# Performance work log

Hardware: AMD Instinct MI355X
Metric: run time of the kernel (lower is better)

The kernel has to match this reference:

```python
import jax, jax.numpy as jnp
import numpy as np
import math

ENC_MAX = 64
DEC_MAX = 128


def _tran_mask(M):
    # faithful reconstruction of self.tran and self.mask buffers
    fs = math.log(DEC_MAX / (DEC_MAX + ENC_MAX))  # fixed_shift_p
    fe = math.log(ENC_MAX / (DEC_MAX + ENC_MAX))  # fixed_emit_p
    i = np.arange(M)[:, None]
    j = np.arange(M)[None, :]
    tran = np.where(i + j < M, (M - (i + j) - 1) * fs + fe, 0.0).astype(np.float32)
    # mask_br: -inf where i+j >= M (anti-diagonal i+j==M-1 stays 0)
    mask = np.where(i + j >= M, -np.inf, 0.0).astype(np.float32)
    return jnp.asarray(tran), jnp.asarray(mask)


def _lstm(xs, Wih, Whh, bih, bhh):
    # xs: [L, in]; torch LSTM gate order i,f,g,o; batch=1 handled as unbatched
    H = Whh.shape[1]
    def step(carry, xt):
        h, c = carry
        g = Wih @ xt + bih + Whh @ h + bhh  # [4H]
        i, f, gg, o = jnp.split(g, 4)
        c = jax.nn.sigmoid(f) * c + jax.nn.sigmoid(i) * jnp.tanh(gg)
        h = jax.nn.sigmoid(o) * jnp.tanh(c)
        return (h, c), h
    _, hs = jax.lax.scan(step, (jnp.zeros((H,), xs.dtype), jnp.zeros((H,), xs.dtype)), xs)
    return hs  # [L, H]


def setup_inputs() -> dict:
    key = jax.random.key(0)
    ks = jax.random.split(key, 16)
    V, E, H, K, T = 32000, 100, 512, ENC_MAX, DEC_MAX
    def p(k, shape, scale):
        return jax.random.normal(k, shape, dtype=jnp.float32) * scale
    return {
        "x": jax.random.randint(ks[0], (1, K), 0, V),
        "y": jax.random.randint(ks[1], (1, T), 0, V),
        "emb": p(ks[2], (V, E), 0.1),
        "enc_Wih": p(ks[3], (4 * H, E), 1.0 / np.sqrt(E)),
        "enc_Whh": p(ks[4], (4 * H, H), 1.0 / np.sqrt(H)),
        "enc_bih": jnp.zeros((4 * H,), jnp.float32),
        "enc_bhh": jnp.zeros((4 * H,), jnp.float32),
        "dec_Wih": p(ks[5], (4 * H, E), 1.0 / np.sqrt(E)),
        "dec_Whh": p(ks[6], (4 * H, H), 1.0 / np.sqrt(H)),
        "dec_bih": jnp.zeros((4 * H,), jnp.float32),
        "dec_bhh": jnp.zeros((4 * H,), jnp.float32),
        "Weh": p(ks[7], (E, 2 * H), 1.0 / np.sqrt(2 * H)),  # emit_hidden
        "beh": jnp.zeros((E,), jnp.float32),
        "Wem": p(ks[8], (V, E), 1.0 / np.sqrt(E)),  # emit
        "bem": jnp.zeros((V,), jnp.float32),
    }


def reference(x, y, emb, enc_Wih, enc_Whh, enc_bih, enc_bhh,
              dec_Wih, dec_Whh, dec_bih, dec_bhh, Weh, beh, Wem, bem):
    K = x.shape[1]
    T = y.shape[1]
    x_emb = emb[x[0]]            # [K, E]
    y_emb = emb[y[0]]            # [T, E]
    Eenc = _lstm(x_emb, enc_Wih, enc_Whh, enc_bih, enc_bhh)  # [K, H]
    D = _lstm(y_emb, dec_Wih, dec_Whh, dec_bih, dec_bhh)     # [T, H]

    tran, mask = _tran_mask(ENC_MAX)
    tranm = tran[ENC_MAX - K:, :K] + mask[ENC_MAX - K:, :K]  # [K, K]

    # emissions for all steps at once (joint = cat(E, D_{t-1}) -> relu -> emit -> log_softmax -> gather word_t)
    H = Eenc.shape[1]
    We_E, We_D = Weh[:, :H], Weh[:, H:]
    hpre = jax.nn.relu(Eenc @ We_E.T + (D[:T - 1] @ We_D.T)[:, None, :] + beh)  # [T-1, K, E]
    logits = jnp.einsum('tke,ve->tkv', hpre, Wem) + bem                          # [T-1, K, V]
    words = y[0, 1:]                                                             # [T-1]
    gathered = jnp.take_along_axis(logits, words[:, None, None], axis=2)[..., 0]  # [T-1, K]
    emission = gathered - jax.scipy.special.logsumexp(logits, axis=2)             # [T-1, K]

    def step(pre_alpha, em_t):
        scores = pre_alpha[:, None] + tranm            # [K(i), K(j)]
        mx = jnp.max(scores, axis=0)                   # [K]
        ind = jnp.argmax(scores, axis=0).astype(jnp.int32)
        mx = jnp.flip(mx)                              # self.flip
        ind = jnp.flip(ind)
        new = mx + em_t
        return new, ind

    pre_alpha, inds = jax.lax.scan(step, jnp.zeros((K,), jnp.float32), emission)
    indices = jnp.concatenate([jnp.zeros((1, K), jnp.int32), inds], axis=0)  # [T, K]

    val = pre_alpha[K - 1]  # align_last

    def bstep(ind, idx_row):
        nind = idx_row[ind]
        return nind, nind
    _, alignments = jax.lax.scan(bstep, jnp.int32(K - 1), indices, reverse=True)  # [T]
    return alignments, val
```

## Files before the change

### kernel.cpp

```cpp
#include <hip/hip_runtime.h>


#define K_ENC 64
#define HID   512
#define EMB   100
#define VOC   32000
#define G4    2048

typedef __attribute__((ext_vector_type(8))) short  short8;
typedef __attribute__((ext_vector_type(4))) float  f32x4;
typedef __attribute__((ext_vector_type(4))) int    i32x4;
typedef unsigned long long u64;

#define LOG2E 1.4426950408889634f
#define LN2   0.6931471805599453f

__device__ __forceinline__ unsigned short f2bf(float f) {
  union { float f; unsigned u; } x; x.f = f;
  unsigned r = x.u + 0x7FFFu + ((x.u >> 16) & 1u);
  return (unsigned short)(r >> 16);
}

__device__ __forceinline__ float fast_sigmoid(float x) {
  return __builtin_amdgcn_rcpf(1.f + __builtin_amdgcn_exp2f(-LOG2E * x));
}
__device__ __forceinline__ float fast_tanh(float x) {
  return 1.f - 2.f * __builtin_amdgcn_rcpf(1.f + __builtin_amdgcn_exp2f(2.f * LOG2E * x));
}

#define OFF_PAD   0
#define OFF_HBUF  256
#define OFF_G0E   4352
#define OFF_G0D   135424
#define OFF_EENC  395520
#define OFF_D     428288
#define OFF_EWE   493312
#define OFF_DWD   499712
#define OFF_BEM   512412
#define OFF_SUM   544412
#define OFF_EM    552540
#define OFF_WEM   560668

__global__ void kZero(float* __restrict__ ws) {
  int gid = blockIdx.x * 256 + threadIdx.x;
  if (gid < 4352) ws[gid] = 0.f;
  else if (gid < 4352 + 127 * 64) ws[OFF_SUM + gid - 4352] = 0.f;
}

__global__ __launch_bounds__(256) void kG0(const int* __restrict__ x, const int* __restrict__ y,
                    const float* __restrict__ emb,
                    const float* __restrict__ eWih, const float* __restrict__ ebih,
                    const float* __restrict__ ebhh,
                    const float* __restrict__ dWih, const float* __restrict__ dbih,
                    const float* __restrict__ dbhh,
                    float* __restrict__ ws) {
  int gid = blockIdx.x * 256 + threadIdx.x;
  const int enc_total = K_ENC * G4;
  if (gid >= enc_total + 127 * G4) return;
  bool enc = gid < enc_total;
  int loc = enc ? gid : gid - enc_total;
  int t = loc >> 11, r = loc & (G4 - 1);
  int tok = enc ? x[t] : y[t];
  const float* Wr = (enc ? eWih : dWih) + r * EMB;
  const float* er = emb + tok * EMB;
  float s = 0.f;
  #pragma unroll 4
  for (int e = 0; e < EMB; ++e) s += er[e] * Wr[e];
  s += enc ? (ebih[r] + ebhh[r]) : (dbih[r] + dbhh[r]);
  ws[(enc ? OFF_G0E : OFF_G0D) + t * G4 + r] = s;
}

__global__ __launch_bounds__(256) void kWemPrep(const float* __restrict__ Wem,
                                               const float* __restrict__ bem,
                                               float* __restrict__ ws) {
  int gid = blockIdx.x * 256 + threadIdx.x;
  int vt = gid >> 11;
  int kb = (gid >> 9) & 3;
  int L  = (gid >> 3) & 63;
  int j  = gid & 7;
  int v = vt * 16 + (L & 15);
  int k = kb * 32 + ((L >> 4) << 3) + j;
  float val = (k < EMB) ? Wem[v * EMB + k] : 0.f;
  ((unsigned short*)(ws + OFF_WEM))[gid] = f2bf(val);
  if (gid < VOC) ws[OFF_BEM + gid] = bem[gid] * LOG2E;
}

#define STEP_GUARD 16384

__global__ __launch_bounds__(512, 2) void kLstm(const float* __restrict__ eWhh,
                                                const float* __restrict__ dWhh,
                                                float* __restrict__ ws) {
  const int grp = blockIdx.x >> 5;
  const int wg  = blockIdx.x & 31;
  const float* __restrict__ Whh = grp ? dWhh : eWhh;
  const float* __restrict__ G0  = ws + (grp ? OFF_G0D : OFF_G0E);
  float* hs = ws + (grp ? OFF_D : OFF_EENC);
  u64* hb = (u64*)(ws + OFF_HBUF) + grp * 1024;
  const int steps = grp ? 127 : K_ENC;
  const int tid = threadIdx.x;
  const int jl = tid >> 5, sub = tid & 31;
  const int j = wg * 16 + jl;
  __shared__ float h_lds[32 * 20];

  float cst = 0.f;
  for (int t = 0; t < steps; ++t) {
    float4 w4[16];
    #pragma unroll
    for (int g = 0; g < 4; ++g)
      #pragma unroll
      for (int q = 0; q < 4; ++q)
        w4[g * 4 + q] = *(const float4*)&Whh[(g * HID + j) * HID + sub * 16 + q * 4];
    float g0i = G0[t * G4 + j];
    float g0f = G0[t * G4 + HID + j];
    float g0g = G0[t * G4 + 2 * HID + j];
    float g0o = G0[t * G4 + 3 * HID + j];
    if (tid < 256) {
      const u64* src = hb + (t & 1) * 512 + tid * 2;
      i32x4 v;
      int guard = 0;
      for (;;) {
        asm volatile("global_load_dwordx4 %0, %1, off sc0 sc1\n\t"
                     "s_waitcnt vmcnt(0)"
                     : "=v"(v) : "v"(src) : "memory");
        if ((v[1] == t && v[3] == t) || ++guard >= STEP_GUARD) break;
        __builtin_amdgcn_s_sleep(1);
      }
      int k0 = tid * 2, k1 = k0 + 1;
      union { int u; float f; } c0, c1; c0.u = v[0]; c1.u = v[2];
      h_lds[(k0 >> 4) * 20 + (k0 & 15)] = c0.f;
      h_lds[(k1 >> 4) * 20 + (k1 & 15)] = c1.f;
    }
    __syncthreads();
    float h[16];
    #pragma unroll
    for (int kk = 0; kk < 16; ++kk) h[kk] = h_lds[sub * 20 + kk];
    float p0 = 0.f, p1 = 0.f, p2 = 0.f, p3 = 0.f;
    #pragma unroll
    for (int q = 0; q < 4; ++q) {
      p0 += w4[0+q].x*h[q*4+0] + w4[0+q].y*h[q*4+1] + w4[0+q].z*h[q*4+2] + w4[0+q].w*h[q*4+3];
      p1 += w4[4+q].x*h[q*4+0] + w4[4+q].y*h[q*4+1] + w4[4+q].z*h[q*4+2] + w4[4+q].w*h[q*4+3];
      p2 += w4[8+q].x*h[q*4+0] + w4[8+q].y*h[q*4+1] + w4[8+q].z*h[q*4+2] + w4[8+q].w*h[q*4+3];
      p3 += w4[12+q].x*h[q*4+0] + w4[12+q].y*h[q*4+1] + w4[12+q].z*h[q*4+2] + w4[12+q].w*h[q*4+3];
    }
    #pragma unroll
    for (int d = 1; d <= 16; d <<= 1) {
      p0 += __shfl_xor(p0, d); p1 += __shfl_xor(p1, d);
      p2 += __shfl_xor(p2, d); p3 += __shfl_xor(p3, d);
    }
    float si = fast_sigmoid(g0i + p0);
    float sf = fast_sigmoid(g0f + p1);
    float gG = fast_tanh(g0g + p2);
    float so = fast_sigmoid(g0o + p3);
    cst = sf * cst + si * gG;
    float hn = so * fast_tanh(cst);
    if (sub == 0) {
      union { float f; unsigned u; } hu; hu.f = hn;
      u64 pack = ((u64)(unsigned)(t + 1) << 32) | (u64)hu.u;
      atomicExch(&hb[((t + 1) & 1) * 512 + j], pack);
      hs[t * HID + j] = hn;
    }
    __syncthreads();
  }
}

__global__ __launch_bounds__(256) void kProj(const float* __restrict__ Weh,
                                             const float* __restrict__ beh,
                                             float* __restrict__ ws) {
  int bid = blockIdx.x;
  bool enc = bid < K_ENC;
  int row = enc ? bid : bid - K_ENC;
  const float* in = ws + (enc ? OFF_EENC : OFF_D) + row * HID;
  __shared__ float sin_[HID];
  int tid = threadIdx.x;
  sin_[tid] = in[tid]; sin_[tid + 256] = in[tid + 256];
  __syncthreads();
  if (tid < EMB) {
    const float* wr = Weh + tid * 1024 + (enc ? 0 : HID);
    float s = 0.f;
    #pragma unroll 4
    for (int h = 0; h < HID; ++h) s += sin_[h] * wr[h];
    if (!enc) s += beh[tid];
    ws[(enc ? OFF_EWE : OFF_DWD) + row * EMB + tid] = s * LOG2E;
  }
}

__global__ __launch_bounds__(256) void kLogits(float* __restrict__ ws) {
  const int t = blockIdx.x >> 2;
  const int chunk = blockIdx.x & 3;
  const int tid = threadIdx.x;
  const int lane = tid & 63;
  const int wv = tid >> 6;
  const int quad = lane >> 4, l15 = lane & 15;
  __shared__ __align__(16) unsigned short A[64 * 128];
  const float* EWe = ws + OFF_EWE;
  const float* DWd = ws + OFF_DWD + t * EMB;
  for (int idx = tid; idx < 64 * 128; idx += 256) {
    int m = idx >> 7, k = idx & 127;
    float hv = 0.f;
    if (k < EMB) { float s = EWe[m * EMB + k] + DWd[k]; hv = s > 0.f ? s : 0.f; }
    A[idx] = f2bf(hv);
  }
  __syncthreads();
  short8 af[4][4];
  #pragma unroll
  for (int mt = 0; mt < 4; ++mt)
    #pragma unroll
    for (int kb = 0; kb < 4; ++kb)
      af[mt][kb] = *(const short8*)&A[(mt * 16 + l15) * 128 + kb * 32 + quad * 8];
  const unsigned short* wem = (const unsigned short*)(ws + OFF_WEM);
  const float* bem_s = ws + OFF_BEM;
  float rs[4][4];
  #pragma unroll
  for (int a = 0; a < 4; ++a)
    #pragma unroll
    for (int b = 0; b < 4; ++b) rs[a][b] = 0.f;
  int vt = chunk * 500 + wv;
  short8 nb0, nb1, nb2, nb3; float nbi;
  nb0 = *(const short8*)&wem[(vt * 4 + 0) * 512 + lane * 8];
  nb1 = *(const short8*)&wem[(vt * 4 + 1) * 512 + lane * 8];
  nb2 = *(const short8*)&wem[(vt * 4 + 2) * 512 + lane * 8];
  nb3 = *(const short8*)&wem[(vt * 4 + 3) * 512 + lane * 8];
  nbi = bem_s[vt * 16 + l15];
  for (int ii = wv; ii < 500; ii += 4) {
    short8 cb0 = nb0, cb1 = nb1, cb2 = nb2, cb3 = nb3;
    float cbi = nbi;
    int nvt = vt + 4;
    if (ii + 4 < 500) {
      nb0 = *(const short8*)&wem[(nvt * 4 + 0) * 512 + lane * 8];
      nb1 = *(const short8*)&wem[(nvt * 4 + 1) * 512 + lane * 8];
      nb2 = *(const short8*)&wem[(nvt * 4 + 2) * 512 + lane * 8];
      nb3 = *(const short8*)&wem[(nvt * 4 + 3) * 512 + lane * 8];
      nbi = bem_s[nvt * 16 + l15];
    }
    f32x4 acc[4];
    #pragma unroll
    for (int mt = 0; mt < 4; ++mt) acc[mt] = (f32x4){cbi, cbi, cbi, cbi};
    #pragma unroll
    for (int mt = 0; mt < 4; ++mt) {
      acc[mt] = __builtin_amdgcn_mfma_f32_16x16x32_bf16(af[mt][0], cb0, acc[mt], 0, 0, 0);
      acc[mt] = __builtin_amdgcn_mfma_f32_16x16x32_bf16(af[mt][1], cb1, acc[mt], 0, 0, 0);
      acc[mt] = __builtin_amdgcn_mfma_f32_16x16x32_bf16(af[mt][2], cb2, acc[mt], 0, 0, 0);
      acc[mt] = __builtin_amdgcn_mfma_f32_16x16x32_bf16(af[mt][3], cb3, acc[mt], 0, 0, 0);
    }
    #pragma unroll
    for (int mt = 0; mt < 4; ++mt)
      #pragma unroll
      for (int r = 0; r < 4; ++r)
        rs[mt][r] += __builtin_amdgcn_exp2f(acc[mt][r]);
    vt = nvt;
  }
  #pragma unroll
  for (int d = 1; d < 16; d <<= 1)
    #pragma unroll
    for (int mt = 0; mt < 4; ++mt)
      #pragma unroll
      for (int r = 0; r < 4; ++r)
        rs[mt][r] += __shfl_xor(rs[mt][r], d);
  if (l15 == 0) {
    float* sum = ws + OFF_SUM + t * 64;
    #pragma unroll
    for (int mt = 0; mt < 4; ++mt)
      #pragma unroll
      for (int r = 0; r < 4; ++r)
        atomicAdd(&sum[mt * 16 + quad * 4 + r], rs[mt][r]);
  }
}

__global__ __launch_bounds__(256) void kEmission(const int* __restrict__ y,
                                                 const float* __restrict__ Wem,
                                                 float* __restrict__ ws) {
  int gid = blockIdx.x * 256 + threadIdx.x;
  if (gid >= 127 * 64) return;
  int t = gid >> 6, m = gid & 63;
  const float* ew = ws + OFF_EWE + m * EMB;
  const float* dw = ws + OFF_DWD + t * EMB;
  int wt = y[t + 1];
  const float* wr = Wem + wt * EMB;
  float s = ws[OFF_BEM + wt];
  #pragma unroll 4
  for (int e = 0; e < EMB; ++e) {
    float h = ew[e] + dw[e];
    h = h > 0.f ? h : 0.f;
    s += h * wr[e];
  }
  ws[OFF_EM + gid] = LN2 * (s - __builtin_amdgcn_logf(ws[OFF_SUM + gid]));
}

__global__ __launch_bounds__(256) void kViterbi(const float* __restrict__ ws, float* __restrict__ out) {
  __shared__ float em_lds[127 * 64];
  __shared__ int   inds[128 * 64];
  __shared__ float sval;
  const int tid = threadIdx.x;
  for (int i = tid; i < 127 * 64; i += 256) em_lds[i] = ws[OFF_EM + i];
  if (tid < 64) inds[tid] = 0;
  __syncthreads();
  if (tid < 64) {
    const int j = tid;
    const float fs = -0.4054651081081644f;
    const float fe = -1.0986122886681098f;
    float pa = 0.f;
    float emnext = em_lds[j];
    for (int t = 0; t < 127; ++t) {
      float emc = emnext;
      if (t < 126) emnext = em_lds[(t + 1) * 64 + j];
      float v = fmaf(-fs, (float)j, pa);
      int idx = j;
      #pragma unroll
      for (int d = 1; d < 64; d <<= 1) {
        float vv = __shfl_up(v, d);
        int   ii = __shfl_up(idx, d);
        bool cur = v > vv;
        v   = cur ? v : vv;
        idx = cur ? idx : ii;
      }
      pa = v + fe + fs * (float)j + emc;
      inds[(t + 1) * 64 + j] = idx;
    }
    if (j == 63) sval = pa;
  }
  __syncthreads();
  if (tid == 0) {
    int ind = 63;
    for (int t = 127; t >= 0; --t) {
      ind = inds[t * 64 + ind];
      out[t] = (float)ind;
    }
    out[128] = sval;
  }
}

extern "C" void kernel_launch(void* const* d_in, const int* in_sizes, int n_in,
                              void* d_out, int out_size, void* d_ws, size_t ws_size,
                              hipStream_t stream) {
  const int*   x    = (const int*)d_in[0];
  const int*   y    = (const int*)d_in[1];
  const float* emb  = (const float*)d_in[2];
  const float* eWih = (const float*)d_in[3];
  const float* eWhh = (const float*)d_in[4];
  const float* ebih = (const float*)d_in[5];
  const float* ebhh = (const float*)d_in[6];
  const float* dWih = (const float*)d_in[7];
  const float* dWhh = (const float*)d_in[8];
  const float* dbih = (const float*)d_in[9];
  const float* dbhh = (const float*)d_in[10];
  const float* Weh  = (const float*)d_in[11];
  const float* beh  = (const float*)d_in[12];
  const float* Wem  = (const float*)d_in[13];
  const float* bem  = (const float*)d_in[14];
  float* ws  = (float*)d_ws;
  float* out = (float*)d_out;

  hipLaunchKernelGGL(kZero,     dim3(49),    dim3(256), 0, stream, ws);
  hipLaunchKernelGGL(kG0,       dim3(1528),  dim3(256), 0, stream, x, y, emb, eWih, ebih, ebhh, dWih, dbih, dbhh, ws);
  hipLaunchKernelGGL(kWemPrep,  dim3(16000), dim3(256), 0, stream, Wem, bem, ws);
  hipLaunchKernelGGL(kLstm,     dim3(64),    dim3(512), 0, stream, eWhh, dWhh, ws);
  hipLaunchKernelGGL(kProj,     dim3(191),   dim3(256), 0, stream, Weh, beh, ws);
  hipLaunchKernelGGL(kLogits,   dim3(508),   dim3(256), 0, stream, ws);
  hipLaunchKernelGGL(kEmission, dim3(32),    dim3(256), 0, stream, y, Wem, ws);
  hipLaunchKernelGGL(kViterbi,  dim3(1),     dim3(256), 0, stream, ws, out);
}
```

Baseline: 510.3 us.

## Merge prep kernels into one launch and fuse emit projection into LSTM loop

The zero, input-gate and Wem-conversion kernels become one launch that dispatches on block index. The separate projection kernel is removed: idle waves in each LSTM block compute the Weh projection of the previous step's hidden state from shared memory, at the cost of one extra loop iteration. This removes two kernel launches and a dependent pass over the hidden states. It adds a little work inside the serial recurrence, which could lengthen the critical path.

```diff
diff --git a/kernel.cpp b/kernel.cpp
--- a/kernel.cpp
+++ b/kernel.cpp
@@ -41,79 +41,98 @@
 #define OFF_EM    552540
 #define OFF_WEM   560668
 
-__global__ void kZero(float* __restrict__ ws) {
-  int gid = blockIdx.x * 256 + threadIdx.x;
-  if (gid < 4352) ws[gid] = 0.f;
-  else if (gid < 4352 + 127 * 64) ws[OFF_SUM + gid - 4352] = 0.f;
-}
-
-__global__ __launch_bounds__(256) void kG0(const int* __restrict__ x, const int* __restrict__ y,
+#define PREP_WEM_BLKS 16000
+#define PREP_G0_BLKS  1528
+__global__ __launch_bounds__(256) void kPrep(const int* __restrict__ x, const int* __restrict__ y,
                     const float* __restrict__ emb,
                     const float* __restrict__ eWih, const float* __restrict__ ebih,
                     const float* __restrict__ ebhh,
                     const float* __restrict__ dWih, const float* __restrict__ dbih,
                     const float* __restrict__ dbhh,
+                    const float* __restrict__ Wem, const float* __restrict__ bem,
                     float* __restrict__ ws) {
-  int gid = blockIdx.x * 256 + threadIdx.x;
-  const int enc_total = K_ENC * G4;
-  if (gid >= enc_total + 127 * G4) return;
-  bool enc = gid < enc_total;
-  int loc = enc ? gid : gid - enc_total;
-  int t = loc >> 11, r = loc & (G4 - 1);
-  int tok = enc ? x[t] : y[t];
-  const float* Wr = (enc ? eWih : dWih) + r * EMB;
-  const float* er = emb + tok * EMB;
-  float s = 0.f;
-  #pragma unroll 4
-  for (int e = 0; e < EMB; ++e) s += er[e] * Wr[e];
-  s += enc ? (ebih[r] + ebhh[r]) : (dbih[r] + dbhh[r]);
-  ws[(enc ? OFF_G0E : OFF_G0D) + t * G4 + r] = s;
-}
-
-__global__ __launch_bounds__(256) void kWemPrep(const float* __restrict__ Wem,
-                                               const float* __restrict__ bem,
-                                               float* __restrict__ ws) {
-  int gid = blockIdx.x * 256 + threadIdx.x;
-  int vt = gid >> 11;
-  int kb = (gid >> 9) & 3;
-  int L  = (gid >> 3) & 63;
-  int j  = gid & 7;
-  int v = vt * 16 + (L & 15);
-  int k = kb * 32 + ((L >> 4) << 3) + j;
-  float val = (k < EMB) ? Wem[v * EMB + k] : 0.f;
-  ((unsigned short*)(ws + OFF_WEM))[gid] = f2bf(val);
-  if (gid < VOC) ws[OFF_BEM + gid] = bem[gid] * LOG2E;
+  const int b = blockIdx.x;
+  const int tid = threadIdx.x;
+  if (b < PREP_WEM_BLKS) {
+    int gid = b * 256 + tid;
+    int vt = gid >> 11;
+    int kb = (gid >> 9) & 3;
+    int L  = (gid >> 3) & 63;
+    int j  = gid & 7;
+    int v = vt * 16 + (L & 15);
+    int k = kb * 32 + ((L >> 4) << 3) + j;
+    float val = (k < EMB) ? Wem[v * EMB + k] : 0.f;
+    ((unsigned short*)(ws + OFF_WEM))[gid] = f2bf(val);
+    if (gid < VOC) ws[OFF_BEM + gid] = bem[gid] * LOG2E;
+  } else if (b < PREP_WEM_BLKS + PREP_G0_BLKS) {
+    int gid = (b - PREP_WEM_BLKS) * 256 + tid;
+    const int enc_total = K_ENC * G4;
+    if (gid >= enc_total + 127 * G4) return;
+    bool enc = gid < enc_total;
+    int loc = enc ? gid : gid - enc_total;
+    int t = loc >> 11, r = loc & (G4 - 1);
+    int tok = enc ? x[t] : y[t];
+    const float* Wr = (enc ? eWih : dWih) + r * EMB;
+    const float* er = emb + tok * EMB;
+    float s = 0.f;
+    #pragma unroll 4
+    for (int e = 0; e < EMB; ++e) s += er[e] * Wr[e];
+    s += enc ? (ebih[r] + ebhh[r]) : (dbih[r] + dbhh[r]);
+    ws[(enc ? OFF_G0E : OFF_G0D) + t * G4 + r] = s;
+  } else {
+    int gid = (b - PREP_WEM_BLKS - PREP_G0_BLKS) * 256 + tid;
+    if (gid < 4352) ws[gid] = 0.f;
+    else if (gid < 4352 + 127 * 64) ws[OFF_SUM + gid - 4352] = 0.f;
+  }
 }
 
 #define STEP_GUARD 16384
 
 __global__ __launch_bounds__(512, 2) void kLstm(const float* __restrict__ eWhh,
                                                 const float* __restrict__ dWhh,
+                                                const float* __restrict__ Weh,
+                                                const float* __restrict__ beh,
                                                 float* __restrict__ ws) {
   const int grp = blockIdx.x >> 5;
   const int wg  = blockIdx.x & 31;
   const float* __restrict__ Whh = grp ? dWhh : eWhh;
   const float* __restrict__ G0  = ws + (grp ? OFF_G0D : OFF_G0E);
   float* hs = ws + (grp ? OFF_D : OFF_EENC);
+  float* proj = ws + (grp ? OFF_DWD : OFF_EWE);
   u64* hb = (u64*)(ws + OFF_HBUF) + grp * 1024;
   const int steps = grp ? 127 : K_ENC;
   const int tid = threadIdx.x;
   const int jl = tid >> 5, sub = tid & 31;
   const int j = wg * 16 + jl;
+  const int wv = tid >> 6, lane = tid & 63;
   __shared__ float h_lds[32 * 20];
 
+  const int e = wg * 4 + (wv - 4);
+  const bool do_proj = (wv >= 4) && (e < EMB);
+  float4 pw0 = {0.f, 0.f, 0.f, 0.f}, pw1 = {0.f, 0.f, 0.f, 0.f};
+  float pbias = 0.f;
+  if (do_proj) {
+    const float* wr = Weh + e * 1024 + (grp ? HID : 0) + lane * 8;
+    pw0 = *(const float4*)wr;
+    pw1 = *(const float4*)(wr + 4);
+    if (grp) pbias = beh[e];
+  }
+
   float cst = 0.f;
-  for (int t = 0; t < steps; ++t) {
+  for (int t = 0; t <= steps; ++t) {
     float4 w4[16];
-    #pragma unroll
-    for (int g = 0; g < 4; ++g)
-      #pragma unroll
-      for (int q = 0; q < 4; ++q)
-        w4[g * 4 + q] = *(const float4*)&Whh[(g * HID + j) * HID + sub * 16 + q * 4];
-    float g0i = G0[t * G4 + j];
-    float g0f = G0[t * G4 + HID + j];
-    float g0g = G0[t * G4 + 2 * HID + j];
-    float g0o = G0[t * G4 + 3 * HID + j];
+    float g0i = 0.f, g0f = 0.f, g0g = 0.f, g0o = 0.f;
+    if (t < steps) {
+      #pragma unroll
+      for (int g = 0; g < 4; ++g)
+        #pragma unroll
+        for (int q = 0; q < 4; ++q)
+          w4[g * 4 + q] = *(const float4*)&Whh[(g * HID + j) * HID + sub * 16 + q * 4];
+      g0i = G0[t * G4 + j];
+      g0f = G0[t * G4 + HID + j];
+      g0g = G0[t * G4 + 2 * HID + j];
+      g0o = G0[t * G4 + 3 * HID + j];
+    }
     if (tid < 256) {
       const u64* src = hb + (t & 1) * 512 + tid * 2;
       i32x4 v;
@@ -131,56 +150,53 @@
       h_lds[(k1 >> 4) * 20 + (k1 & 15)] = c1.f;
     }
     __syncthreads();
-    float h[16];
-    #pragma unroll
-    for (int kk = 0; kk < 16; ++kk) h[kk] = h_lds[sub * 20 + kk];
-    float p0 = 0.f, p1 = 0.f, p2 = 0.f, p3 = 0.f;
-    #pragma unroll
-    for (int q = 0; q < 4; ++q) {
-      p0 += w4[0+q].x*h[q*4+0] + w4[0+q].y*h[q*4+1] + w4[0+q].z*h[q*4+2] + w4[0+q].w*h[q*4+3];
-      p1 += w4[4+q].x*h[q*4+0] + w4[4+q].y*h[q*4+1] + w4[4+q].z*h[q*4+2] + w4[4+q].w*h[q*4+3];
-      p2 += w4[8+q].x*h[q*4+0] + w4[8+q].y*h[q*4+1] + w4[8+q].z*h[q*4+2] + w4[8+q].w*h[q*4+3];
-      p3 += w4[12+q].x*h[q*4+0] + w4[12+q].y*h[q*4+1] + w4[12+q].z*h[q*4+2] + w4[12+q].w*h[q*4+3];
-    }
-    #pragma unroll
-    for (int d = 1; d <= 16; d <<= 1) {
-      p0 += __shfl_xor(p0, d); p1 += __shfl_xor(p1, d);
-      p2 += __shfl_xor(p2, d); p3 += __shfl_xor(p3, d);
-    }
-    float si = fast_sigmoid(g0i + p0);
-    float sf = fast_sigmoid(g0f + p1);
-    float gG = fast_tanh(g0g + p2);
-    float so = fast_sigmoid(g0o + p3);
-    cst = sf * cst + si * gG;
-    float hn = so * fast_tanh(cst);
-    if (sub == 0) {
-      union { float f; unsigned u; } hu; hu.f = hn;
-      u64 pack = ((u64)(unsigned)(t + 1) << 32) | (u64)hu.u;
-      atomicExch(&hb[((t + 1) & 1) * 512 + j], pack);
-      hs[t * HID + j] = hn;
+    if (t >= 1 && do_proj) {
+      float p = 0.f;
+      #pragma unroll
+      for (int i = 0; i < 4; ++i) {
+        int k = lane * 8 + i;
+        p += ((const float*)&pw0)[i] * h_lds[(k >> 4) * 20 + (k & 15)];
+      }
+      #pragma unroll
+      for (int i = 4; i < 8; ++i) {
+        int k = lane * 8 + i;
+        p += ((const float*)&pw1)[i - 4] * h_lds[(k >> 4) * 20 + (k & 15)];
+      }
+      #pragma unroll
+      for (int d = 1; d < 64; d <<= 1) p += __shfl_xor(p, d);
+      if (lane == 0) proj[(t - 1) * EMB + e] = (p + pbias) * LOG2E;
+    }
+    if (t < steps) {
+      float h[16];
+      #pragma unroll
+      for (int kk = 0; kk < 16; ++kk) h[kk] = h_lds[sub * 20 + kk];
+      float p0 = 0.f, p1 = 0.f, p2 = 0.f, p3 = 0.f;
+      #pragma unroll
+      for (int q = 0; q < 4; ++q) {
+        p0 += w4[0+q].x*h[q*4+0] + w4[0+q].y*h[q*4+1] + w4[0+q].z*h[q*4+2] + w4[0+q].w*h[q*4+3];
+        p1 += w4[4+q].x*h[q*4+0] + w4[4+q].y*h[q*4+1] + w4[4+q].z*h[q*4+2] + w4[4+q].w*h[q*4+3];
+        p2 += w4[8+q].x*h[q*4+0] + w4[8+q].y*h[q*4+1] + w4[8+q].z*h[q*4+2] + w4[8+q].w*h[q*4+3];
+        p3 += w4[12+q].x*h[q*4+0] + w4[12+q].y*h[q*4+1] + w4[12+q].z*h[q*4+2] + w4[12+q].w*h[q*4+3];
+      }
+      #pragma unroll
+      for (int d = 1; d <= 16; d <<= 1) {
+        p0 += __shfl_xor(p0, d); p1 += __shfl_xor(p1, d);
+        p2 += __shfl_xor(p2, d); p3 += __shfl_xor(p3, d);
+      }
+      float si = fast_sigmoid(g0i + p0);
+      float sf = fast_sigmoid(g0f + p1);
+      float gG = fast_tanh(g0g + p2);
+      float so = fast_sigmoid(g0o + p3);
+      cst = sf * cst + si * gG;
+      float hn = so * fast_tanh(cst);
+      if (sub == 0) {
+        union { float f; unsigned u; } hu; hu.f = hn;
+        u64 pack = ((u64)(unsigned)(t + 1) << 32) | (u64)hu.u;
+        atomicExch(&hb[((t + 1) & 1) * 512 + j], pack);
+        hs[t * HID + j] = hn;
+      }
     }
     __syncthreads();
-  }
-}
-
-__global__ __launch_bounds__(256) void kProj(const float* __restrict__ Weh,
-                                             const float* __restrict__ beh,
-                                             float* __restrict__ ws) {
-  int bid = blockIdx.x;
-  bool enc = bid < K_ENC;
-  int row = enc ? bid : bid - K_ENC;
-  const float* in = ws + (enc ? OFF_EENC : OFF_D) + row * HID;
-  __shared__ float sin_[HID];
-  int tid = threadIdx.x;
-  sin_[tid] = in[tid]; sin_[tid + 256] = in[tid + 256];
-  __syncthreads();
-  if (tid < EMB) {
-    const float* wr = Weh + tid * 1024 + (enc ? 0 : HID);
-    float s = 0.f;
-    #pragma unroll 4
-    for (int h = 0; h < HID; ++h) s += sin_[h] * wr[h];
-    if (!enc) s += beh[tid];
-    ws[(enc ? OFF_EWE : OFF_DWD) + row * EMB + tid] = s * LOG2E;
   }
 }
 
@@ -350,11 +366,9 @@
   float* ws  = (float*)d_ws;
   float* out = (float*)d_out;
 
-  hipLaunchKernelGGL(kZero,     dim3(49),    dim3(256), 0, stream, ws);
-  hipLaunchKernelGGL(kG0,       dim3(1528),  dim3(256), 0, stream, x, y, emb, eWih, ebih, ebhh, dWih, dbih, dbhh, ws);
-  hipLaunchKernelGGL(kWemPrep,  dim3(16000), dim3(256), 0, stream, Wem, bem, ws);
-  hipLaunchKernelGGL(kLstm,     dim3(64),    dim3(512), 0, stream, eWhh, dWhh, ws);
-  hipLaunchKernelGGL(kProj,     dim3(191),   dim3(256), 0, stream, Weh, beh, ws);
+  hipLaunchKernelGGL(kPrep,     dim3(PREP_WEM_BLKS + PREP_G0_BLKS + 49), dim3(256), 0, stream,
+                     x, y, emb, eWih, ebih, ebhh, dWih, dbih, dbhh, Wem, bem, ws);
+  hipLaunchKernelGGL(kLstm,     dim3(64),    dim3(512), 0, stream, eWhh, dWhh, Weh, beh, ws);
   hipLaunchKernelGGL(kLogits,   dim3(508),   dim3(256), 0, stream, ws);
   hipLaunchKernelGGL(kEmission, dim3(32),    dim3(256), 0, stream, y, Wem, ws);
   hipLaunchKernelGGL(kViterbi,  dim3(1),     dim3(256), 0, stream, ws, out);
```

New measurement: 676.1 us. 1.32x slower.
